# Performance work log

Measured on AMD Instinct MI355X. Metric: run time of the kernel, lower is better.

Reference implementation:

```python
import jax, jax.numpy as jnp
import numpy as np

N = 50000       # nodes
E = 1_200_000   # directed edges (avg degree 24)
IN_F = 128
C = 64          # CL1_F hidden width
K = 3           # Chebyshev order
OUT_F = 2
EPS = 1e-5      # BatchNorm eps (torch default)


def setup_inputs() -> dict:
    key = jax.random.key(0)
    ks = jax.random.split(key, 8)
    s = 0.1
    x = jax.random.normal(ks[0], (N, IN_F), dtype=jnp.float32)
    edge_index = jax.random.randint(ks[1], (2, E), 0, N, dtype=jnp.int32)
    W1 = jax.random.normal(ks[2], (K, IN_F, C), dtype=jnp.float32) * s
    b1 = jnp.zeros((C,), jnp.float32)
    W_rest = jax.random.normal(ks[3], (9, K, C, C), dtype=jnp.float32) * s
    b_rest = jnp.zeros((9, C), jnp.float32)
    gamma = jnp.ones((10, C), jnp.float32)
    beta = jnp.zeros((10, C), jnp.float32)
    lin_w = jax.random.normal(ks[4], (C, OUT_F), dtype=jnp.float32) * s
    lin_b = jnp.zeros((OUT_F,), jnp.float32)
    return dict(x=x, edge_index=edge_index, W1=W1, b1=b1, W_rest=W_rest,
                b_rest=b_rest, gamma=gamma, beta=beta, lin_w=lin_w, lin_b=lin_b)


def _cheb_norm(edge_index):
    # PyG ChebConv normalization with lambda_max=2, sym Laplacian, unit edge weights:
    # L_hat = 2L/lambda_max - I = -D^{-1/2} A D^{-1/2} (diagonal becomes 0).
    row, col = edge_index[0], edge_index[1]
    deg = jax.ops.segment_sum(jnp.ones((E,), jnp.float32), row, num_segments=N)
    dinv = jnp.where(deg > 0, jax.lax.rsqrt(jnp.maximum(deg, 1.0)), 0.0)
    w = -dinv[row] * dinv[col]  # per-edge weight of L_hat
    return row, col, w


def _cheb_conv(x, W, b, row, col, w):
    # Chebyshev recursion: Tx_0 = x, Tx_1 = L_hat x, Tx_k = 2 L_hat Tx_{k-1} - Tx_{k-2}
    Lhat = lambda v: jax.ops.segment_sum(w[:, None] * v[col], row, num_segments=N)
    Tx0 = x
    out = Tx0 @ W[0]
    Tx1 = Lhat(x)
    out = out + Tx1 @ W[1]
    for k in range(2, W.shape[0]):
        Tx2 = 2.0 * Lhat(Tx1) - Tx0
        out = out + Tx2 @ W[k]
        Tx0, Tx1 = Tx1, Tx2
    return out + b


def _bn(x, g, b):
    # BatchNorm1d over nodes (training-mode batch statistics, biased var)
    mu = x.mean(axis=0)
    var = ((x - mu) ** 2).mean(axis=0)
    return g * (x - mu) * jax.lax.rsqrt(var + EPS) + b


def reference(x, edge_index, W1, b1, W_rest, b_rest, gamma, beta, lin_w, lin_b):
    row, col, w = _cheb_norm(edge_index)
    h = _bn(jax.nn.relu(_cheb_conv(x, W1, b1, row, col, w)), gamma[0], beta[0])
    for i in range(9):  # convs 2..10 (structurally identical, stacked params)
        h = _bn(jax.nn.relu(_cheb_conv(h, W_rest[i], b_rest[i], row, col, w)),
                gamma[i + 1], beta[i + 1])
    return h @ lin_w + lin_b
```

## Files before the change

### kernel.cpp

```cpp
#include <hip/hip_runtime.h>
#include <hip/hip_bf16.h>

#define N_NODES 50000
#define N_EDGES 1200000
#define EPS_BN 1e-5f
#define NB 1024
#define RPB 49
#define CAP 2048

typedef __attribute__((ext_vector_type(8))) short short8;
typedef __attribute__((ext_vector_type(4))) float f32x4;

union U16x8 { uint4 u; short8 s; };

__device__ __forceinline__ float lo2f(unsigned int u){ return __uint_as_float(u << 16); }
__device__ __forceinline__ float hi2f(unsigned int u){ return __uint_as_float(u & 0xffff0000u); }
__device__ __forceinline__ float b2f(unsigned short u){ return __uint_as_float(((unsigned int)u) << 16); }
__device__ __forceinline__ unsigned short f2b(float f){
  __hip_bfloat16 b = __float2bfloat16(f);
  return __builtin_bit_cast(unsigned short, b);
}

__global__ void binA(const int* __restrict__ row, const int* __restrict__ col,
                     int* __restrict__ bcnt, int* __restrict__ tmp, int E){
  __shared__ int hist[NB];
  __shared__ int base[NB];
  for (int i=threadIdx.x; i<NB; i+=256) hist[i] = 0;
  __syncthreads();
  int e0 = blockIdx.x*4096;
  int r_[16], c_[16];
  #pragma unroll
  for (int k=0;k<16;k++){
    int e = e0 + k*256 + threadIdx.x;
    if (e < E){
      r_[k] = row[e]; c_[k] = col[e];
      atomicAdd(&hist[r_[k]/RPB], 1);
    } else r_[k] = -1;
  }
  __syncthreads();
  for (int i=threadIdx.x; i<NB; i+=256){
    int cnt = hist[i];
    base[i] = cnt ? atomicAdd(&bcnt[i], cnt) : 0;
    hist[i] = 0;
  }
  __syncthreads();
  #pragma unroll
  for (int k=0;k<16;k++){
    if (r_[k] >= 0){
      int b = r_[k]/RPB;
      int lr = r_[k] - b*RPB;
      int p = base[b] + atomicAdd(&hist[b], 1);
      tmp[(size_t)b*CAP + p] = (lr << 16) | c_[k];
    }
  }
}

__global__ void scan1024(const int* __restrict__ bcnt, int* __restrict__ bbase,
                         int* __restrict__ offs, int n, int E){
  __shared__ int tmp[NB];
  int i = threadIdx.x;
  int v = bcnt[i];
  tmp[i] = v;
  __syncthreads();
  for (int off=1; off<NB; off<<=1){
    int t = (i >= off) ? tmp[i-off] : 0;
    __syncthreads();
    tmp[i] += t;
    __syncthreads();
  }
  bbase[i] = tmp[i] - v;
  if (i == 0) offs[n] = E;
}

__global__ void binB(const int* __restrict__ bcnt, const int* __restrict__ bbase,
                     const int* __restrict__ tmp,
                     int* __restrict__ offs, float* __restrict__ dinv,
                     float* __restrict__ rdeg, int* __restrict__ ep, int n){
  __shared__ int cnt[RPB];
  __shared__ int roff[RPB];
  int b = blockIdx.x;
  int r0 = b*RPB;
  int m = bcnt[b];
  size_t tbase = (size_t)b*CAP;
  for (int i=threadIdx.x; i<RPB; i+=256) cnt[i] = 0;
  __syncthreads();
  for (int t=threadIdx.x; t<m; t+=256)
    atomicAdd(&cnt[tmp[tbase+t] >> 16], 1);
  __syncthreads();
  if (threadIdx.x == 0){
    int acc = bbase[b];
    #pragma unroll
    for (int i=0;i<RPB;i++){ roff[i] = acc; acc += cnt[i]; }
  }
  __syncthreads();
  if (threadIdx.x < RPB){
    int r = r0 + threadIdx.x;
    if (r < n){
      offs[r] = roff[threadIdx.x];
      int d = cnt[threadIdx.x];
      dinv[r] = (d>0) ? rsqrtf((float)d) : 0.f;
      rdeg[r] = (d>0) ? sqrtf((float)d) : 0.f;
    }
  }
  __syncthreads();
  for (int i=threadIdx.x; i<RPB; i+=256) cnt[i] = 0;
  __syncthreads();
  for (int t=threadIdx.x; t<m; t+=256){
    int v = tmp[tbase+t];
    int lr = v >> 16;
    int p = roff[lr] + atomicAdd(&cnt[lr], 1);
    ep[p] = v & 0xFFFF;
  }
}

__global__ void transpose_w(const float* __restrict__ W1, const float* __restrict__ Wr,
                            unsigned short* __restrict__ WTh,
                            unsigned short* __restrict__ WTl,
                            unsigned short* __restrict__ BCT){
  int t = blockIdx.x*256 + threadIdx.x;
  if (t < 8192){
    int c = t/128, k = t%128;
    float val = W1[(size_t)k*64 + c] - W1[(size_t)(256+k)*64 + c];
    unsigned short h = f2b(val);
    WTh[t] = h; WTl[t] = f2b(val - b2f(h));
  } else if (t < 118784){
    int u = t - 8192;
    int L = u/12288, r2 = u%12288;
    int c = r2/192, kk = r2%192;
    int seg = kk/64, f = kk%64;
    const float* WL = Wr + (size_t)L*12288;
    float val;
    if (seg==0)      val = WL[(size_t)f*64 + c] - WL[(size_t)(128+f)*64 + c];
    else if (seg==1) val = WL[(size_t)(64+f)*64 + c];
    else             val = 2.f * WL[(size_t)(128+f)*64 + c];
    unsigned short h = f2b(val);
    WTh[t] = h; WTl[t] = f2b(val - b2f(h));
  } else if (t < 135168){
    int u = t - 118784;
    int j = u/128, k = u%128;
    float val = (j < 64) ? W1[(size_t)(128+k)*64 + j]
                         : 2.f * W1[(size_t)(256+k)*64 + (j-64)];
    BCT[u] = f2b(val);
  }
}

__device__ __forceinline__ void spmm_acc8(uint4 u, float* a){
  a[0] += lo2f(u.x);
  a[1] += hi2f(u.x);
  a[2] += lo2f(u.y);
  a[3] += hi2f(u.y);
  a[4] += lo2f(u.z);
  a[5] += hi2f(u.z);
  a[6] += lo2f(u.w);
  a[7] += hi2f(u.w);
}

template<int MODE>
__global__ void spmm64(const int* __restrict__ offs, const int* __restrict__ ep,
                       const float* __restrict__ dinv,
                       const unsigned short* __restrict__ src,
                       const unsigned short* __restrict__ padd,
                       unsigned short* __restrict__ dst, int n){
  int lane = threadIdx.x & 63;
  int wv = threadIdx.x >> 6;
  int lr = lane >> 3;
  int li = lane & 7;
  int row = (blockIdx.x*4 + wv)*8 + lr;
  int s = 0, e = 0;
  if (row < n){ s = offs[row]; e = offs[row+1]; }
  float a[8];
  #pragma unroll
  for (int c=0;c<8;c++) a[c]=0.f;
  const int fb = li*8;
  int j = s;
  for (; j+4 <= e; j += 4){
    int c0 = ep[j+0];
    int c1 = ep[j+1];
    int c2 = ep[j+2];
    int c3 = ep[j+3];
    uint4 u0 = *(const uint4*)(src + (size_t)c0*64 + fb);
    uint4 u1 = *(const uint4*)(src + (size_t)c1*64 + fb);
    uint4 u2 = *(const uint4*)(src + (size_t)c2*64 + fb);
    uint4 u3 = *(const uint4*)(src + (size_t)c3*64 + fb);
    spmm_acc8(u0, a);
    spmm_acc8(u1, a);
    spmm_acc8(u2, a);
    spmm_acc8(u3, a);
  }
  for (; j < e; ++j){
    uint4 u = *(const uint4*)(src + (size_t)ep[j]*64 + fb);
    spmm_acc8(u, a);
  }
  if (row < n){
    float dv = dinv[row];
    float uv[8];
    #pragma unroll
    for (int c=0;c<8;c++) uv[c] = -dv * a[c];
    if (MODE == 2){
      uint4 pu = *(const uint4*)(padd + (size_t)row*64 + fb);
      float pv[8] = {lo2f(pu.x),hi2f(pu.x),lo2f(pu.y),hi2f(pu.y),
                     lo2f(pu.z),hi2f(pu.z),lo2f(pu.w),hi2f(pu.w)};
      #pragma unroll
      for (int c=0;c<8;c++) uv[c] = dv*(pv[c] + uv[c]);
    } else if (MODE == 1){
      #pragma unroll
      for (int c=0;c<8;c++) uv[c] = dv*uv[c];
    }
    uint4 o;
    unsigned int* op = (unsigned int*)&o;
    #pragma unroll
    for (int p=0;p<4;p++)
      op[p] = (unsigned int)f2b(uv[2*p]) | ((unsigned int)f2b(uv[2*p+1]) << 16);
    *(uint4*)(dst + (size_t)row*64 + fb) = o;
  }
}

__global__ void gemm1_l1(const float* __restrict__ x, const unsigned short* __restrict__ BCT,
                         const float* __restrict__ dinv,
                         unsigned short* __restrict__ pb, unsigned short* __restrict__ qs,
                         int n){
  __shared__ unsigned short wlds[128*128];
  #pragma unroll
  for (int c0=0; c0<2048; c0+=256){
    int c = c0 + threadIdx.x;
    int col = c >> 4, k8 = c & 15;
    uint4 v = *(const uint4*)(BCT + (size_t)col*128 + k8*8);
    int byte = (col*128 + k8*8)*2;
    byte ^= (col & 7) << 4;
    *(uint4*)((char*)wlds + byte) = v;
  }
  int lane = threadIdx.x & 63;
  int wv = threadIdx.x >> 6;
  int mrow = lane & 15;
  int kg = lane >> 4;
  int brow = blockIdx.x*64 + wv*16;
  int m = brow + mrow;
  bool mv = m < n;

  U16x8 af[4];
  #pragma unroll
  for (int kk=0;kk<4;kk++){
    int koff = kk*32 + kg*8;
    unsigned int* hp = (unsigned int*)&af[kk].u;
    if (mv){
      const float* gp = x + (size_t)m*128 + koff;
      float4 v0 = *(const float4*)gp;
      float4 v1 = *(const float4*)(gp+4);
      float g[8] = {v0.x,v0.y,v0.z,v0.w,v1.x,v1.y,v1.z,v1.w};
      #pragma unroll
      for (int p=0;p<4;p++)
        hp[p] = (unsigned int)f2b(g[2*p]) | ((unsigned int)f2b(g[2*p+1]) << 16);
    } else {
      af[kk].u = make_uint4(0,0,0,0);
    }
  }
  __syncthreads();

  f32x4 acc[8];
  #pragma unroll
  for (int t=0;t<8;t++) acc[t] = f32x4{0.f,0.f,0.f,0.f};
  #pragma unroll
  for (int kk=0;kk<4;kk++){
    int koff = kk*32 + kg*8;
    #pragma unroll
    for (int t=0;t<8;t++){
      int col = t*16 + mrow;
      int byte = (col*128 + koff)*2;
      byte ^= (col & 7) << 4;
      U16x8 b;
      b.u = *(const uint4*)((const char*)wlds + byte);
      acc[t] = __builtin_amdgcn_mfma_f32_16x16x32_bf16(af[kk].s, b.s, acc[t], 0, 0, 0);
    }
  }

  #pragma unroll
  for (int t=0;t<8;t++){
    int col = t*16 + mrow;
    #pragma unroll
    for (int i=0;i<4;i++){
      int r = brow + kg*4 + i;
      if (r < n){
        if (col < 64) pb[(size_t)r*64 + col] = f2b(acc[t][i]);
        else          qs[(size_t)r*64 + col - 64] = f2b(dinv[r]*acc[t][i]);
      }
    }
  }
}

__global__ void gemm2_l1(const float* __restrict__ x,
                         const unsigned short* __restrict__ ATh,
                         const unsigned short* __restrict__ ATl,
                         const unsigned short* __restrict__ su,
                         const float* __restrict__ bias,
                         float* __restrict__ out, float* __restrict__ stats, int n){
  __shared__ unsigned short wlds[2*64*128];
  __shared__ float ssum[64];
  __shared__ float ssq[64];
  if (threadIdx.x < 64){ ssum[threadIdx.x] = 0.f; ssq[threadIdx.x] = 0.f; }
  #pragma unroll
  for (int c0=0; c0<2048; c0+=256){
    int c = c0 + threadIdx.x;
    int plane = c >> 10;
    int r = c & 1023;
    int col = r >> 4, k8 = r & 15;
    const unsigned short* srcp = (plane ? ATl : ATh) + (size_t)col*128 + k8*8;
    uint4 v = *(const uint4*)srcp;
    int byte = ((plane*64 + col)*128 + k8*8)*2;
    byte ^= (col & 7) << 4;
    *(uint4*)((char*)wlds + byte) = v;
  }
  int lane = threadIdx.x & 63;
  int wv = threadIdx.x >> 6;
  int mrow = lane & 15;
  int kg = lane >> 4;
  int brow = blockIdx.x*64 + wv*16;
  int m = brow + mrow;
  bool mv = m < n;

  U16x8 afh[4], afl[4];
  #pragma unroll
  for (int kk=0;kk<4;kk++){
    int koff = kk*32 + kg*8;
    unsigned int* hp = (unsigned int*)&afh[kk].u;
    unsigned int* lp = (unsigned int*)&afl[kk].u;
    if (mv){
      const float* gp = x + (size_t)m*128 + koff;
      float4 v0 = *(const float4*)gp;
      float4 v1 = *(const float4*)(gp+4);
      float g[8] = {v0.x,v0.y,v0.z,v0.w,v1.x,v1.y,v1.z,v1.w};
      #pragma unroll
      for (int p=0;p<4;p++){
        unsigned short h0 = f2b(g[2*p]),  h1 = f2b(g[2*p+1]);
        unsigned short l0 = f2b(g[2*p] - b2f(h0)), l1 = f2b(g[2*p+1] - b2f(h1));
        hp[p] = (unsigned int)h0 | ((unsigned int)h1 << 16);
        lp[p] = (unsigned int)l0 | ((unsigned int)l1 << 16);
      }
    } else {
      afh[kk].u = make_uint4(0,0,0,0);
      afl[kk].u = make_uint4(0,0,0,0);
    }
  }
  __syncthreads();

  f32x4 acc[4];
  #pragma unroll
  for (int t=0;t<4;t++) acc[t] = f32x4{0.f,0.f,0.f,0.f};
  #pragma unroll
  for (int kk=0;kk<4;kk++){
    int koff = kk*32 + kg*8;
    #pragma unroll
    for (int t=0;t<4;t++){
      int col = t*16 + mrow;
      int byteh = (col*128 + koff)*2;          byteh ^= (col & 7) << 4;
      int bytel = ((64 + col)*128 + koff)*2;   bytel ^= (col & 7) << 4;
      U16x8 bh, bl;
      bh.u = *(const uint4*)((const char*)wlds + byteh);
      bl.u = *(const uint4*)((const char*)wlds + bytel);
      acc[t] = __builtin_amdgcn_mfma_f32_16x16x32_bf16(afh[kk].s, bh.s, acc[t], 0, 0, 0);
      acc[t] = __builtin_amdgcn_mfma_f32_16x16x32_bf16(afh[kk].s, bl.s, acc[t], 0, 0, 0);
      acc[t] = __builtin_amdgcn_mfma_f32_16x16x32_bf16(afl[kk].s, bh.s, acc[t], 0, 0, 0);
    }
  }

  #pragma unroll
  for (int t=0;t<4;t++){
    int col = t*16 + mrow;
    float bsv = bias[col];
    float s = 0.f, sq = 0.f;
    #pragma unroll
    for (int i=0;i<4;i++){
      int r = brow + kg*4 + i;
      if (r < n){
        float v = acc[t][i] + b2f(su[(size_t)r*64 + col]) + bsv;
        v = fmaxf(v, 0.f);
        out[(size_t)r*64 + col] = v;
        s += v; sq += v*v;
      }
    }
    s  += __shfl_xor(s, 16);  sq += __shfl_xor(sq, 16);
    s  += __shfl_xor(s, 32);  sq += __shfl_xor(sq, 32);
    if (kg == 0){
      atomicAdd(&ssum[col], s);
      atomicAdd(&ssq[col], sq);
    }
  }
  __syncthreads();
  if (threadIdx.x < 64){
    float* sl = stats + (blockIdx.x & 15)*128;
    atomicAdd(&sl[threadIdx.x], ssum[threadIdx.x]);
    atomicAdd(&sl[64+threadIdx.x], ssq[threadIdx.x]);
  }
}

__global__ void gemm_mfma64(const float* __restrict__ A0f,
                            const float* __restrict__ scsh,
                            const unsigned short* __restrict__ A1,
                            const unsigned short* __restrict__ A2,
                            const float* __restrict__ rdeg,
                            const unsigned short* __restrict__ WTh,
                            const unsigned short* __restrict__ WTl,
                            const float* __restrict__ bias,
                            float* __restrict__ out,
                            float* __restrict__ stats, int n){
  constexpr int SEGF = 64;
  constexpr int K = 192;
  __shared__ unsigned short wlds[2*64*SEGF];
  __shared__ float ssum[64];
  __shared__ float ssq[64];
  __shared__ float sc_l[64];
  __shared__ float sh_l[64];
  if (threadIdx.x < 64){
    ssum[threadIdx.x] = 0.f; ssq[threadIdx.x] = 0.f;
    sc_l[threadIdx.x] = scsh[threadIdx.x];
    sh_l[threadIdx.x] = scsh[64 + threadIdx.x];
  }

  int lane = threadIdx.x & 63;
  int wv = threadIdx.x >> 6;
  int mrow = lane & 15;
  int kg = lane >> 4;
  int brow = blockIdx.x*64 + wv*16;
  int m = brow + mrow;
  bool mv = m < n;
  float rm = mv ? rdeg[m] : 0.f;

  f32x4 acc[4];
  #pragma unroll
  for (int t=0;t<4;t++) acc[t] = f32x4{0.f,0.f,0.f,0.f};

  #pragma unroll
  for (int seg=0; seg<3; ++seg){
    #pragma unroll
    for (int c0=0; c0<1024; c0+=256){
      int c = c0 + threadIdx.x;
      int plane = c >> 9;
      int r = c & 511;
      int col = r >> 3, k8 = r & 7;
      const unsigned short* srcp = (plane ? WTl : WTh) + (size_t)col*K + seg*SEGF + k8*8;
      uint4 v = *(const uint4*)srcp;
      int byte = ((plane*64 + col)*SEGF + k8*8)*2;
      byte ^= (col & 7) << 4;
      *(uint4*)((char*)wlds + byte) = v;
    }
    U16x8 afh[2], afl[2];
    #pragma unroll
    for (int kk=0; kk<2; ++kk){
      int koff = kk*32 + kg*8;
      if (seg==0){
        float y[8];
        if (mv){
          const float* gp = A0f + (size_t)m*SEGF + koff;
          float4 v0 = *(const float4*)gp;
          float4 v1 = *(const float4*)(gp+4);
          float g[8] = {v0.x,v0.y,v0.z,v0.w,v1.x,v1.y,v1.z,v1.w};
          #pragma unroll
          for (int i=0;i<8;i++){
            int f = koff + i;
            y[i] = fmaf(g[i], sc_l[f], sh_l[f]);
          }
        } else {
          #pragma unroll
          for (int i=0;i<8;i++) y[i] = 0.f;
        }
        unsigned int* hp = (unsigned int*)&afh[kk].u;
        unsigned int* lp = (unsigned int*)&afl[kk].u;
        #pragma unroll
        for (int p=0;p<4;p++){
          unsigned short h0 = f2b(y[2*p]),  h1 = f2b(y[2*p+1]);
          unsigned short l0 = f2b(y[2*p] - b2f(h0)), l1 = f2b(y[2*p+1] - b2f(h1));
          hp[p] = (unsigned int)h0 | ((unsigned int)h1 << 16);
          lp[p] = (unsigned int)l0 | ((unsigned int)l1 << 16);
        }
      } else if (seg==1){
        unsigned int* hp = (unsigned int*)&afh[kk].u;
        if (mv){
          uint4 u = *(const uint4*)(A1 + (size_t)m*SEGF + koff);
          float g[8] = {lo2f(u.x),hi2f(u.x),lo2f(u.y),hi2f(u.y),
                        lo2f(u.z),hi2f(u.z),lo2f(u.w),hi2f(u.w)};
          #pragma unroll
          for (int p=0;p<4;p++)
            hp[p] = (unsigned int)f2b(rm*g[2*p]) | ((unsigned int)f2b(rm*g[2*p+1]) << 16);
        } else afh[kk].u = make_uint4(0,0,0,0);
      } else {
        if (mv) afh[kk].u = *(const uint4*)(A2 + (size_t)m*SEGF + koff);
        else    afh[kk].u = make_uint4(0,0,0,0);
      }
    }
    __syncthreads();
    #pragma unroll
    for (int kk=0; kk<2; ++kk){
      #pragma unroll
      for (int t=0;t<4;t++){
        int col = t*16 + mrow;
        int koff = kk*32 + kg*8;
        int byteh = (col*SEGF + koff)*2;          byteh ^= (col & 7) << 4;
        int bytel = ((64 + col)*SEGF + koff)*2;   bytel ^= (col & 7) << 4;
        U16x8 bh, bl;
        bh.u = *(const uint4*)((const char*)wlds + byteh);
        bl.u = *(const uint4*)((const char*)wlds + bytel);
        acc[t] = __builtin_amdgcn_mfma_f32_16x16x32_bf16(afh[kk].s, bh.s, acc[t], 0, 0, 0);
        acc[t] = __builtin_amdgcn_mfma_f32_16x16x32_bf16(afh[kk].s, bl.s, acc[t], 0, 0, 0);
        if (seg==0)
          acc[t] = __builtin_amdgcn_mfma_f32_16x16x32_bf16(afl[kk].s, bh.s, acc[t], 0, 0, 0);
      }
    }
    __syncthreads();
  }

  #pragma unroll
  for (int t=0;t<4;t++){
    int col = t*16 + mrow;
    float bsv = bias[col];
    float s = 0.f, sq = 0.f;
    #pragma unroll
    for (int i=0;i<4;i++){
      int r = brow + kg*4 + i;
      if (r < n){
        float v = fmaxf(acc[t][i] + bsv, 0.f);
        out[(size_t)r*64 + col] = v;
        s += v; sq += v*v;
      }
    }
    s  += __shfl_xor(s, 16);  sq += __shfl_xor(sq, 16);
    s  += __shfl_xor(s, 32);  sq += __shfl_xor(sq, 32);
    if (kg == 0){
      atomicAdd(&ssum[col], s);
      atomicAdd(&ssq[col], sq);
    }
  }
  __syncthreads();
  if (threadIdx.x < 64){
    float* sl = stats + (blockIdx.x & 15)*128;
    atomicAdd(&sl[threadIdx.x], ssum[threadIdx.x]);
    atomicAdd(&sl[64+threadIdx.x], ssq[threadIdx.x]);
  }
}

__global__ void bn_scale(const float* __restrict__ g_in, const float* __restrict__ dinv,
                         unsigned short* __restrict__ hs,
                         const float* __restrict__ stats, float* __restrict__ scsh,
                         const float* __restrict__ gamma, const float* __restrict__ beta,
                         int n){
  __shared__ float red[128];
  __shared__ float sc[64], sh[64];
  int tid = threadIdx.x;
  if (tid < 128){
    float s = 0.f;
    #pragma unroll
    for (int r=0;r<16;r++) s += stats[r*128 + tid];
    red[tid] = s;
  }
  __syncthreads();
  if (tid < 64){
    float inv_n = 1.f/(float)n;
    float mu = red[tid]*inv_n;
    float var = red[64+tid]*inv_n - mu*mu;
    float a = gamma[tid]*rsqrtf(var + EPS_BN);
    sc[tid] = a;
    sh[tid] = beta[tid] - mu*a;
    if (blockIdx.x == 0){
      scsh[tid] = a;
      scsh[64+tid] = sh[tid];
    }
  }
  __syncthreads();
  int t = blockIdx.x*256 + tid;
  if (t >= n*8) return;
  int fb = (t & 7)*8;
  int node = t >> 3;
  float dv = dinv[node];
  const float* gp = g_in + (size_t)node*64 + fb;
  float4 v0 = *(const float4*)gp;
  float4 v1 = *(const float4*)(gp + 4);
  float vv[8] = {v0.x, v0.y, v0.z, v0.w, v1.x, v1.y, v1.z, v1.w};
  uint4 o;
  unsigned int* op = (unsigned int*)&o;
  #pragma unroll
  for (int p=0;p<4;p++){
    int f0 = fb + 2*p, f1 = f0 + 1;
    float y0 = dv * fmaf(vv[2*p],   sc[f0], sh[f0]);
    float y1 = dv * fmaf(vv[2*p+1], sc[f1], sh[f1]);
    op[p] = (unsigned int)f2b(y0) | ((unsigned int)f2b(y1) << 16);
  }
  ((uint4*)hs)[t] = o;
}

__global__ void final_linear_bn(const float* __restrict__ g_in,
                                const float* __restrict__ stats,
                                const float* __restrict__ gamma, const float* __restrict__ beta,
                                const float* __restrict__ w, const float* __restrict__ b,
                                float* __restrict__ out, int n){
  __shared__ float red[128];
  __shared__ float sc[64], sh[64];
  int tid = threadIdx.x;
  if (tid < 128){
    float s = 0.f;
    #pragma unroll
    for (int r=0;r<16;r++) s += stats[r*128 + tid];
    red[tid] = s;
  }
  __syncthreads();
  if (tid < 64){
    float inv_n = 1.f/(float)n;
    float mu = red[tid]*inv_n;
    float var = red[64+tid]*inv_n - mu*mu;
    float a = gamma[tid]*rsqrtf(var + EPS_BN);
    sc[tid] = a;
    sh[tid] = beta[tid] - mu*a;
  }
  __syncthreads();
  int i = blockIdx.x*256 + tid;
  if (i >= n) return;
  float a0 = b[0], a1 = b[1];
  const float* gp = g_in + (size_t)i*64;
  #pragma unroll
  for (int k=0;k<64;k++){
    float v = fmaf(gp[k], sc[k], sh[k]);
    a0 = fmaf(v, w[k*2+0], a0);
    a1 = fmaf(v, w[k*2+1], a1);
  }
  out[i*2+0] = a0;
  out[i*2+1] = a1;
}

extern "C" void kernel_launch(void* const* d_in, const int* in_sizes, int n_in,
                              void* d_out, int out_size, void* d_ws, size_t ws_size,
                              hipStream_t stream){
  const float* x     = (const float*)d_in[0];
  const int*   ei    = (const int*)d_in[1];
  const float* W1    = (const float*)d_in[2];
  const float* b1    = (const float*)d_in[3];
  const float* Wr    = (const float*)d_in[4];
  const float* br    = (const float*)d_in[5];
  const float* gamma = (const float*)d_in[6];
  const float* beta  = (const float*)d_in[7];
  const float* lw    = (const float*)d_in[8];
  const float* lb    = (const float*)d_in[9];
  const int N = N_NODES, E = N_EDGES;
  const int* row = ei;
  const int* col = ei + E;

  char* ws = (char*)d_ws;
  size_t off = 0;
  auto alloc = [&](size_t bytes)->void*{
    void* p = ws + off; off = (off + bytes + 255) & ~(size_t)255; return p; };
  float*          dinv  = (float*) alloc((size_t)N*4);
  float*          rdeg  = (float*) alloc((size_t)N*4);
  int*            offs  = (int*)   alloc((size_t)(N+1)*4);
  int*            bcnt  = (int*)   alloc(NB*4);
  int*            bbase = (int*)   alloc(NB*4);
  int*            tmp   = (int*)   alloc((size_t)NB*CAP*4);
  int*            ep    = (int*)   alloc((size_t)E*4);
  unsigned short* pb    = (unsigned short*)alloc((size_t)N*64*2);
  unsigned short* qs    = (unsigned short*)alloc((size_t)N*64*2);
  unsigned short* T1s   = (unsigned short*)alloc((size_t)N*64*2);
  unsigned short* Uu    = (unsigned short*)alloc((size_t)N*64*2);
  unsigned short* hs    = (unsigned short*)alloc((size_t)N*64*2);
  float*          gbuf  = (float*) alloc((size_t)N*64*4);
  unsigned short* WTh   = (unsigned short*)alloc((size_t)118784*2);
  unsigned short* WTl   = (unsigned short*)alloc((size_t)118784*2);
  unsigned short* BCT   = (unsigned short*)alloc((size_t)16384*2);
  float*          stats = (float*) alloc((size_t)10*2048*4);
  float*          scsh  = (float*) alloc((size_t)10*128*4);

  hipMemsetAsync(bcnt, 0, NB*4, stream);
  hipMemsetAsync(stats, 0, (size_t)10*2048*4, stream);
  binA<<<(E+4095)/4096, 256, 0, stream>>>(row, col, bcnt, tmp, E);
  scan1024<<<1, NB, 0, stream>>>(bcnt, bbase, offs, N, E);
  binB<<<NB, 256, 0, stream>>>(bcnt, bbase, tmp, offs, dinv, rdeg, ep, N);

  transpose_w<<<(135168+255)/256, 256, 0, stream>>>(W1, Wr, WTh, WTl, BCT);

  int sg = (N+31)/32;
  gemm1_l1<<<(N+63)/64, 256, 0, stream>>>(x, BCT, dinv, pb, qs, N);
  spmm64<2><<<sg, 256, 0, stream>>>(offs, ep, dinv, qs, pb, T1s, N);
  spmm64<0><<<sg, 256, 0, stream>>>(offs, ep, dinv, T1s, nullptr, Uu, N);
  gemm2_l1<<<(N+63)/64, 256, 0, stream>>>(x, WTh, WTl, Uu, b1, gbuf, stats, N);

  for (int L=0; L<9; ++L){
    bn_scale<<<((N*8)+255)/256, 256, 0, stream>>>(gbuf, dinv, hs,
        stats + (size_t)L*2048, scsh + (size_t)L*128,
        gamma + (size_t)L*64, beta + (size_t)L*64, N);
    spmm64<1><<<sg, 256, 0, stream>>>(offs, ep, dinv, hs, nullptr, T1s, N);
    spmm64<0><<<sg, 256, 0, stream>>>(offs, ep, dinv, T1s, nullptr, Uu, N);
    gemm_mfma64<<<(N+63)/64, 256, 0, stream>>>(gbuf, scsh + (size_t)L*128, T1s, Uu, rdeg,
        WTh + 8192 + (size_t)L*12288, WTl + 8192 + (size_t)L*12288,
        br + (size_t)L*64, gbuf, stats + (size_t)(L+1)*2048, N);
  }

  final_linear_bn<<<(N+255)/256, 256, 0, stream>>>(gbuf, stats + (size_t)9*2048,
      gamma + (size_t)9*64, beta + (size_t)9*64, lw, lb, (float*)d_out, N);
}
```

Before: 632.7 us.

## Split SpMM gather into two column-range passes with fp32 partial buffer

Edges of each row are partitioned by source column (below or above the midpoint) during binning, and each SpMM is split into two kernels that gather from only half of the source feature matrix at a time. The aim is to keep each pass's gather working set (about 3.2 MB of bf16 features) resident in cache. The cost is an extra fp32 partial-sum buffer that is written and read back per row (about 12.8 MB each way), plus twice as many kernel launches. Non-temporal stores and loads are used for the partials and the outputs.

```diff
diff --git a/kernel.cpp b/kernel.cpp
--- a/kernel.cpp
+++ b/kernel.cpp
@@ -7,9 +7,11 @@
 #define NB 1024
 #define RPB 49
 #define CAP 2048
+#define MIDCOL 25000
 
 typedef __attribute__((ext_vector_type(8))) short short8;
 typedef __attribute__((ext_vector_type(4))) float f32x4;
+typedef __attribute__((ext_vector_type(4))) unsigned int u32x4;
 
 union U16x8 { uint4 u; short8 s; };
 
@@ -74,42 +76,48 @@
 
 __global__ void binB(const int* __restrict__ bcnt, const int* __restrict__ bbase,
                      const int* __restrict__ tmp,
-                     int* __restrict__ offs, float* __restrict__ dinv,
-                     float* __restrict__ rdeg, int* __restrict__ ep, int n){
-  __shared__ int cnt[RPB];
-  __shared__ int roff[RPB];
+                     int* __restrict__ offs, int* __restrict__ midp,
+                     float* __restrict__ dinv, float* __restrict__ rdeg,
+                     int* __restrict__ ep, int n){
+  __shared__ int cl[RPB], ch[RPB], rl[RPB], rh[RPB];
   int b = blockIdx.x;
   int r0 = b*RPB;
   int m = bcnt[b];
   size_t tbase = (size_t)b*CAP;
-  for (int i=threadIdx.x; i<RPB; i+=256) cnt[i] = 0;
-  __syncthreads();
-  for (int t=threadIdx.x; t<m; t+=256)
-    atomicAdd(&cnt[tmp[tbase+t] >> 16], 1);
+  for (int i=threadIdx.x; i<RPB; i+=256){ cl[i]=0; ch[i]=0; }
+  __syncthreads();
+  for (int t=threadIdx.x; t<m; t+=256){
+    int v = tmp[tbase+t];
+    if ((v & 0xFFFF) < MIDCOL) atomicAdd(&cl[v>>16], 1);
+    else                       atomicAdd(&ch[v>>16], 1);
+  }
   __syncthreads();
   if (threadIdx.x == 0){
     int acc = bbase[b];
     #pragma unroll
-    for (int i=0;i<RPB;i++){ roff[i] = acc; acc += cnt[i]; }
+    for (int i=0;i<RPB;i++){ rl[i] = acc; acc += cl[i]; rh[i] = acc; acc += ch[i]; }
   }
   __syncthreads();
   if (threadIdx.x < RPB){
     int r = r0 + threadIdx.x;
     if (r < n){
-      offs[r] = roff[threadIdx.x];
-      int d = cnt[threadIdx.x];
+      offs[r] = rl[threadIdx.x];
+      midp[r] = rh[threadIdx.x];
+      int d = cl[threadIdx.x] + ch[threadIdx.x];
       dinv[r] = (d>0) ? rsqrtf((float)d) : 0.f;
       rdeg[r] = (d>0) ? sqrtf((float)d) : 0.f;
     }
   }
   __syncthreads();
-  for (int i=threadIdx.x; i<RPB; i+=256) cnt[i] = 0;
+  for (int i=threadIdx.x; i<RPB; i+=256){ cl[i]=0; ch[i]=0; }
   __syncthreads();
   for (int t=threadIdx.x; t<m; t+=256){
     int v = tmp[tbase+t];
-    int lr = v >> 16;
-    int p = roff[lr] + atomicAdd(&cnt[lr], 1);
-    ep[p] = v & 0xFFFF;
+    int lr = v >> 16, c = v & 0xFFFF;
+    int p;
+    if (c < MIDCOL) p = rl[lr] + atomicAdd(&cl[lr], 1);
+    else            p = rh[lr] + atomicAdd(&ch[lr], 1);
+    ep[p] = c;
   }
 }
 
@@ -155,19 +163,17 @@
   a[7] += hi2f(u.w);
 }
 
-template<int MODE>
-__global__ void spmm64(const int* __restrict__ offs, const int* __restrict__ ep,
-                       const float* __restrict__ dinv,
-                       const unsigned short* __restrict__ src,
-                       const unsigned short* __restrict__ padd,
-                       unsigned short* __restrict__ dst, int n){
+__global__ void spmmA(const int* __restrict__ offs, const int* __restrict__ midp,
+                      const int* __restrict__ ep,
+                      const unsigned short* __restrict__ src,
+                      float* __restrict__ part, int n){
   int lane = threadIdx.x & 63;
   int wv = threadIdx.x >> 6;
   int lr = lane >> 3;
   int li = lane & 7;
   int row = (blockIdx.x*4 + wv)*8 + lr;
   int s = 0, e = 0;
-  if (row < n){ s = offs[row]; e = offs[row+1]; }
+  if (row < n){ s = offs[row]; e = midp[row]; }
   float a[8];
   #pragma unroll
   for (int c=0;c<8;c++) a[c]=0.f;
@@ -192,6 +198,58 @@
     spmm_acc8(u, a);
   }
   if (row < n){
+    f32x4 v0 = {a[0], a[1], a[2], a[3]};
+    f32x4 v1 = {a[4], a[5], a[6], a[7]};
+    f32x4* pp = (f32x4*)(part + (size_t)row*64 + fb);
+    __builtin_nontemporal_store(v0, pp);
+    __builtin_nontemporal_store(v1, pp+1);
+  }
+}
+
+template<int MODE>
+__global__ void spmmB(const int* __restrict__ offs, const int* __restrict__ midp,
+                      const int* __restrict__ ep,
+                      const float* __restrict__ dinv,
+                      const unsigned short* __restrict__ src,
+                      const float* __restrict__ part,
+                      const unsigned short* __restrict__ padd,
+                      unsigned short* __restrict__ dst, int n){
+  int lane = threadIdx.x & 63;
+  int wv = threadIdx.x >> 6;
+  int lr = lane >> 3;
+  int li = lane & 7;
+  int row = (blockIdx.x*4 + wv)*8 + lr;
+  int s = 0, e = 0;
+  if (row < n){ s = midp[row]; e = offs[row+1]; }
+  float a[8];
+  #pragma unroll
+  for (int c=0;c<8;c++) a[c]=0.f;
+  const int fb = li*8;
+  int j = s;
+  for (; j+4 <= e; j += 4){
+    int c0 = ep[j+0];
+    int c1 = ep[j+1];
+    int c2 = ep[j+2];
+    int c3 = ep[j+3];
+    uint4 u0 = *(const uint4*)(src + (size_t)c0*64 + fb);
+    uint4 u1 = *(const uint4*)(src + (size_t)c1*64 + fb);
+    uint4 u2 = *(const uint4*)(src + (size_t)c2*64 + fb);
+    uint4 u3 = *(const uint4*)(src + (size_t)c3*64 + fb);
+    spmm_acc8(u0, a);
+    spmm_acc8(u1, a);
+    spmm_acc8(u2, a);
+    spmm_acc8(u3, a);
+  }
+  for (; j < e; ++j){
+    uint4 u = *(const uint4*)(src + (size_t)ep[j]*64 + fb);
+    spmm_acc8(u, a);
+  }
+  if (row < n){
+    const f32x4* pp = (const f32x4*)(part + (size_t)row*64 + fb);
+    f32x4 p0 = __builtin_nontemporal_load(pp);
+    f32x4 p1 = __builtin_nontemporal_load(pp+1);
+    a[0]+=p0.x; a[1]+=p0.y; a[2]+=p0.z; a[3]+=p0.w;
+    a[4]+=p1.x; a[5]+=p1.y; a[6]+=p1.z; a[7]+=p1.w;
     float dv = dinv[row];
     float uv[8];
     #pragma unroll
@@ -206,12 +264,12 @@
       #pragma unroll
       for (int c=0;c<8;c++) uv[c] = dv*uv[c];
     }
-    uint4 o;
-    unsigned int* op = (unsigned int*)&o;
-    #pragma unroll
-    for (int p=0;p<4;p++)
-      op[p] = (unsigned int)f2b(uv[2*p]) | ((unsigned int)f2b(uv[2*p+1]) << 16);
-    *(uint4*)(dst + (size_t)row*64 + fb) = o;
+    u32x4 o;
+    o.x = (unsigned int)f2b(uv[0]) | ((unsigned int)f2b(uv[1]) << 16);
+    o.y = (unsigned int)f2b(uv[2]) | ((unsigned int)f2b(uv[3]) << 16);
+    o.z = (unsigned int)f2b(uv[4]) | ((unsigned int)f2b(uv[5]) << 16);
+    o.w = (unsigned int)f2b(uv[6]) | ((unsigned int)f2b(uv[7]) << 16);
+    __builtin_nontemporal_store(o, (u32x4*)(dst + (size_t)row*64 + fb));
   }
 }
 
@@ -647,6 +705,7 @@
   float*          dinv  = (float*) alloc((size_t)N*4);
   float*          rdeg  = (float*) alloc((size_t)N*4);
   int*            offs  = (int*)   alloc((size_t)(N+1)*4);
+  int*            midp  = (int*)   alloc((size_t)N*4);
   int*            bcnt  = (int*)   alloc(NB*4);
   int*            bbase = (int*)   alloc(NB*4);
   int*            tmp   = (int*)   alloc((size_t)NB*CAP*4);
@@ -656,6 +715,7 @@
   unsigned short* T1s   = (unsigned short*)alloc((size_t)N*64*2);
   unsigned short* Uu    = (unsigned short*)alloc((size_t)N*64*2);
   unsigned short* hs    = (unsigned short*)alloc((size_t)N*64*2);
+  float*          part  = (float*) alloc((size_t)N*64*4);
   float*          gbuf  = (float*) alloc((size_t)N*64*4);
   unsigned short* WTh   = (unsigned short*)alloc((size_t)118784*2);
   unsigned short* WTl   = (unsigned short*)alloc((size_t)118784*2);
@@ -667,22 +727,26 @@
   hipMemsetAsync(stats, 0, (size_t)10*2048*4, stream);
   binA<<<(E+4095)/4096, 256, 0, stream>>>(row, col, bcnt, tmp, E);
   scan1024<<<1, NB, 0, stream>>>(bcnt, bbase, offs, N, E);
-  binB<<<NB, 256, 0, stream>>>(bcnt, bbase, tmp, offs, dinv, rdeg, ep, N);
+  binB<<<NB, 256, 0, stream>>>(bcnt, bbase, tmp, offs, midp, dinv, rdeg, ep, N);
 
   transpose_w<<<(135168+255)/256, 256, 0, stream>>>(W1, Wr, WTh, WTl, BCT);
 
   int sg = (N+31)/32;
   gemm1_l1<<<(N+63)/64, 256, 0, stream>>>(x, BCT, dinv, pb, qs, N);
-  spmm64<2><<<sg, 256, 0, stream>>>(offs, ep, dinv, qs, pb, T1s, N);
-  spmm64<0><<<sg, 256, 0, stream>>>(offs, ep, dinv, T1s, nullptr, Uu, N);
+  spmmA<<<sg, 256, 0, stream>>>(offs, midp, ep, qs, part, N);
+  spmmB<2><<<sg, 256, 0, stream>>>(offs, midp, ep, dinv, qs, part, pb, T1s, N);
+  spmmA<<<sg, 256, 0, stream>>>(offs, midp, ep, T1s, part, N);
+  spmmB<0><<<sg, 256, 0, stream>>>(offs, midp, ep, dinv, T1s, part, nullptr, Uu, N);
   gemm2_l1<<<(N+63)/64, 256, 0, stream>>>(x, WTh, WTl, Uu, b1, gbuf, stats, N);
 
   for (int L=0; L<9; ++L){
     bn_scale<<<((N*8)+255)/256, 256, 0, stream>>>(gbuf, dinv, hs,
         stats + (size_t)L*2048, scsh + (size_t)L*128,
         gamma + (size_t)L*64, beta + (size_t)L*64, N);
-    spmm64<1><<<sg, 256, 0, stream>>>(offs, ep, dinv, hs, nullptr, T1s, N);
-    spmm64<0><<<sg, 256, 0, stream>>>(offs, ep, dinv, T1s, nullptr, Uu, N);
+    spmmA<<<sg, 256, 0, stream>>>(offs, midp, ep, hs, part, N);
+    spmmB<1><<<sg, 256, 0, stream>>>(offs, midp, ep, dinv, hs, part, nullptr, T1s, N);
+    spmmA<<<sg, 256, 0, stream>>>(offs, midp, ep, T1s, part, N);
+    spmmB<0><<<sg, 256, 0, stream>>>(offs, midp, ep, dinv, T1s, part, nullptr, Uu, N);
     gemm_mfma64<<<(N+63)/64, 256, 0, stream>>>(gbuf, scsh + (size_t)L*128, T1s, Uu, rdeg,
         WTh + 8192 + (size_t)L*12288, WTl + 8192 + (size_t)L*12288,
         br + (size_t)L*64, gbuf, stats + (size_t)(L+1)*2048, N);
```

Result: slower. 755.6 us (+19.4%).
